# Performance work log

Measured on AMD Instinct MI355X. Metric: run time of the kernel, lower is better.

The kernel has to match this reference:

```python
import jax, jax.numpy as jnp
import numpy as np

HIDDEN = 768
INTER = 3072
HEADS = 12
HEAD_DIM = INTER // HEADS  # 256
LN_EPS = 1e-6
R_SOFTPLUS_0 = 1.442695041


def setup_inputs() -> dict:
    key = jax.random.key(0)
    ks = jax.random.split(key, 12)
    s = 0.02
    inp = {
        "hidden_states": jax.random.normal(ks[0], (8, 4096, HIDDEN), dtype=jnp.float32),
        "pooling_query": jax.random.normal(ks[1], (1, 1, HIDDEN), dtype=jnp.float32) * s,
        "Wq": jax.random.normal(ks[2], (HIDDEN, INTER), dtype=jnp.float32) * s,
        "bq": jnp.zeros((INTER,), dtype=jnp.float32),
        "Wk": jax.random.normal(ks[3], (HIDDEN, INTER), dtype=jnp.float32) * s,
        "bk": jnp.zeros((INTER,), dtype=jnp.float32),
        "Wv": jax.random.normal(ks[4], (HIDDEN, INTER), dtype=jnp.float32) * s,
        "bv": jnp.zeros((INTER,), dtype=jnp.float32),
        "Wp": jax.random.normal(ks[5], (INTER, HIDDEN), dtype=jnp.float32) * s,
        "bp": jnp.zeros((HIDDEN,), dtype=jnp.float32),
        "per_dim_scale": jnp.zeros((HEAD_DIM,), dtype=jnp.float32),
        "ln_w": jnp.ones((HIDDEN,), dtype=jnp.float32),
        "ln_b": jnp.zeros((HIDDEN,), dtype=jnp.float32),
    }
    return inp


def reference(hidden_states, pooling_query, Wq, bq, Wk, bk, Wv, bv, Wp, bp,
              per_dim_scale, ln_w, ln_b):
    B, S, _ = hidden_states.shape
    dt = hidden_states.dtype

    # Query: single pooling token, identical across batch -> [H, D]
    q = (pooling_query.reshape(1, HIDDEN) @ Wq + bq).reshape(HEADS, HEAD_DIM)
    # PerDimScale: q * (r_softplus0/sqrt(D)) * softplus(per_dim_scale)
    scale = (R_SOFTPLUS_0 / np.sqrt(HEAD_DIM)).astype(np.float32)
    q = q * (scale * jax.nn.softplus(per_dim_scale))

    # K/V projections: [B, S, H, D]
    k = (hidden_states @ Wk + bk).reshape(B, S, HEADS, HEAD_DIM)
    v = (hidden_states @ Wv + bv).reshape(B, S, HEADS, HEAD_DIM)

    # Single-query attention: logits [B, H, S]; scaling=1.0 (scale_logits_by_head_dims=False)
    # logit cap skipped (no_attention_logit_cap=True)
    logits = jnp.einsum("hd,bshd->bhs", q, k)
    attn = jax.nn.softmax(logits.astype(jnp.float32), axis=-1).astype(dt)

    # Weighted sum over seq: [B, H, D] -> concat heads -> [B, H*D]
    ctx = jnp.einsum("bhs,bshd->bhd", attn, v).reshape(B, HEADS * HEAD_DIM)

    out = ctx @ Wp + bp  # [B, HIDDEN]
    # LayerNorm; note the original forward adds ones to ln weight in-place each call,
    # so effective weight for one call is (ln_w + 1).
    mean = jnp.mean(out, axis=-1, keepdims=True)
    var = jnp.var(out, axis=-1, keepdims=True)
    out = (out - mean) * jax.lax.rsqrt(var + LN_EPS) * (ln_w + 1.0) + ln_b

    pooled = out[:, None, :]  # [B, 1, HIDDEN]
    attn_weights = attn[:, :, None, :]  # [B, H, 1, S]
    return pooled, attn_weights
```

## Files before the change

kernel.cpp:

```cpp
#include <hip/hip_runtime.h>
#include <cstdint>
#include <cmath>

#define LN_EPS 1e-6f

#define N_QCH 24u
#define O_QPART 0u
#define O_Q     73728u
#define O_WK    76800u
#define O_BKE   86016u
#define O_PHP   86032u
#define O_PLOG  O_PHP
#define N_SC    32
#define O_PH    (O_PHP + 2359296u)
#define O_CTXP  (O_PH + 73728u)
#define N_CCH   12
#define O_CTX   (O_CTXP + 294912u)
#define O_OUTP  (O_CTX + 24576u)
#define N_ICH   48

__device__ __forceinline__ float waveReduceSum(float v) {
#pragma unroll
    for (int o = 32; o >= 1; o >>= 1) v += __shfl_xor(v, o, 64);
    return v;
}
__device__ __forceinline__ float waveReduceMax(float v) {
#pragma unroll
    for (int o = 32; o >= 1; o >>= 1) v = fmaxf(v, __shfl_xor(v, o, 64));
    return v;
}

__global__ __launch_bounds__(256) void k1_qpart(const float* __restrict__ pq,
                                                const float* __restrict__ Wq,
                                                float* __restrict__ ws) {
    int h = blockIdx.x % 12;
    int ch = blockIdx.x / 12;
    int tid = threadIdx.x;
    int col = h * 256 + tid;
    int c0 = ch * 32;
    float acc = 0.f;
#pragma unroll 8
    for (int i = 0; i < 32; ++i) {
        int c = c0 + i;
        acc += pq[c] * Wq[c * 3072 + col];
    }
    ws[O_QPART + ch * 3072 + col] = acc;
}

__global__ __launch_bounds__(256) void k1b_qreduce(const float* __restrict__ bq,
                                                   const float* __restrict__ pds,
                                                   float* __restrict__ ws) {
    int j = blockIdx.x * 256 + threadIdx.x;
    float acc = bq[j];
#pragma unroll
    for (unsigned ch = 0; ch < N_QCH; ++ch) acc += ws[O_QPART + ch * 3072 + j];
    float x = pds[j & 255];
    float sp = (x > 20.f) ? x : log1pf(expf(x));
    const float scale = 1.442695041f / 16.0f;
    ws[O_Q + j] = acc * scale * sp;
}

__global__ __launch_bounds__(256) void k2_wkeff(const float* __restrict__ Wk,
                                                float* __restrict__ ws) {
    __shared__ float sh[4];
    int tid = threadIdx.x;
    int blk = blockIdx.x;
    int c = blk / 12, h = blk % 12;
    float v = Wk[c * 3072 + h * 256 + tid] * ws[O_Q + h * 256 + tid];
    v = waveReduceSum(v);
    if ((tid & 63) == 0) sh[tid >> 6] = v;
    __syncthreads();
    if (tid == 0) ws[O_WK + c * 12 + h] = sh[0] + sh[1] + sh[2] + sh[3];
}

__global__ __launch_bounds__(256) void k3_logits(const float* __restrict__ hidden,
                                                 float* __restrict__ ws) {
    __shared__ float4 tile4[1536];
    __shared__ float4 wkb4[288];
    int blk = blockIdx.x;
    int half = blk & 1;
    int st = (blk >> 1) & 63;
    int b = blk >> 7;
    int s0 = st * 64;
    const float* hb = hidden + (size_t)(b * 4096 + s0) * 768;
    const float4* wkg4 = reinterpret_cast<const float4*>(ws + O_WK);
    int tid = threadIdx.x;
    int w = tid >> 6, lane = tid & 63;
    float acc[12];
#pragma unroll
    for (int h = 0; h < 12; ++h) acc[h] = 0.f;

    for (int ch = 0; ch < 4; ++ch) {
        int cbase = half * 384 + ch * 96;
        __syncthreads();
        for (int i = tid; i < 288; i += 256) wkb4[i] = wkg4[cbase * 3 + i];
#pragma unroll
        for (int it = 0; it < 6; ++it) {
            int idx = it * 256 + tid;
            int r = idx / 24, j = idx % 24;
            const float4 v = *reinterpret_cast<const float4*>(hb + r * 768 + cbase + j * 4);
            tile4[r * 24 + (j ^ (r & 7))] = v;
        }
        __syncthreads();
#pragma unroll
        for (int jj = 0; jj < 6; ++jj) {
            int jcol = w * 6 + jj;
            float4 x = tile4[lane * 24 + (jcol ^ (lane & 7))];
            const float4* wr = &wkb4[jcol * 12];
            float xc[4] = {x.x, x.y, x.z, x.w};
#pragma unroll
            for (int cc = 0; cc < 4; ++cc) {
                float4 w0 = wr[cc * 3 + 0], w1 = wr[cc * 3 + 1], w2 = wr[cc * 3 + 2];
                acc[0] += xc[cc] * w0.x;  acc[1] += xc[cc] * w0.y;  acc[2]  += xc[cc] * w0.z;  acc[3]  += xc[cc] * w0.w;
                acc[4] += xc[cc] * w1.x;  acc[5] += xc[cc] * w1.y;  acc[6]  += xc[cc] * w1.z;  acc[7]  += xc[cc] * w1.w;
                acc[8] += xc[cc] * w2.x;  acc[9] += xc[cc] * w2.y;  acc[10] += xc[cc] * w2.z;  acc[11] += xc[cc] * w2.w;
            }
        }
    }
    __syncthreads();
    float* red = reinterpret_cast<float*>(tile4);
#pragma unroll
    for (int h = 0; h < 12; ++h) red[(w * 12 + h) * 64 + lane] = acc[h];
    __syncthreads();
    float* plog = ws + O_PLOG;
    for (int idx = tid; idx < 768; idx += 256) {
        int h = idx / 64, r = idx & 63;
        float v = red[(0 + h) * 64 + r] + red[(12 + h) * 64 + r] +
                  red[(24 + h) * 64 + r] + red[(36 + h) * 64 + r];
        plog[(size_t)half * 393216 + (size_t)(b * 12 + h) * 4096 + s0 + r] = v;
    }
}

__global__ __launch_bounds__(256) void k4_softmax(const float* __restrict__ ws,
                                                  float* __restrict__ attn) {
    __shared__ float sh[4];
    int row = blockIdx.x;
    const float4* p0 = reinterpret_cast<const float4*>(ws + O_PLOG + (size_t)row * 4096);
    const float4* p1 = reinterpret_cast<const float4*>(ws + O_PLOG + 393216u + (size_t)row * 4096);
    float* base = attn + (size_t)row * 4096;
    int tid = threadIdx.x;
    float4 x[4];
#pragma unroll
    for (int t = 0; t < 4; ++t) {
        float4 a = p0[t * 256 + tid], c = p1[t * 256 + tid];
        x[t].x = a.x + c.x; x[t].y = a.y + c.y; x[t].z = a.z + c.z; x[t].w = a.w + c.w;
    }
    float m = -1e30f;
#pragma unroll
    for (int t = 0; t < 4; ++t) {
        m = fmaxf(m, fmaxf(fmaxf(x[t].x, x[t].y), fmaxf(x[t].z, x[t].w)));
    }
    m = waveReduceMax(m);
    if ((tid & 63) == 0) sh[tid >> 6] = m;
    __syncthreads();
    m = fmaxf(fmaxf(sh[0], sh[1]), fmaxf(sh[2], sh[3]));
    __syncthreads();
    float s = 0.f;
#pragma unroll
    for (int t = 0; t < 4; ++t) {
        x[t].x = expf(x[t].x - m); x[t].y = expf(x[t].y - m);
        x[t].z = expf(x[t].z - m); x[t].w = expf(x[t].w - m);
        s += x[t].x + x[t].y + x[t].z + x[t].w;
    }
    s = waveReduceSum(s);
    if ((tid & 63) == 0) sh[tid >> 6] = s;
    __syncthreads();
    s = sh[0] + sh[1] + sh[2] + sh[3];
    float inv = 1.0f / s;
#pragma unroll
    for (int t = 0; t < 4; ++t) {
        x[t].x *= inv; x[t].y *= inv; x[t].z *= inv; x[t].w *= inv;
        reinterpret_cast<float4*>(base)[t * 256 + tid] = x[t];
    }
}

__global__ __launch_bounds__(256) void k5_phpart(const float* __restrict__ hidden,
                                                 const float* __restrict__ attn,
                                                 float* __restrict__ ws) {
    int blk = blockIdx.x;
    int sc = blk & 31;
    int ct = (blk >> 5) % 3;
    int b = blk / 96;
    int tid = threadIdx.x;
    int c = ct * 256 + tid;
    int s0 = sc * 128;
    const float* hb = hidden + (size_t)(b * 4096 + s0) * 768 + c;
    const float* ab = attn + (size_t)b * 49152 + s0;
    float acc[12];
#pragma unroll
    for (int h = 0; h < 12; ++h) acc[h] = 0.f;
    for (int g = 0; g < 32; ++g) {
        float x0 = hb[(g * 4 + 0) * 768];
        float x1 = hb[(g * 4 + 1) * 768];
        float x2 = hb[(g * 4 + 2) * 768];
        float x3 = hb[(g * 4 + 3) * 768];
#pragma unroll
        for (int h = 0; h < 12; ++h) {
            const float4 a = *reinterpret_cast<const float4*>(ab + h * 4096 + g * 4);
            acc[h] += a.x * x0 + a.y * x1 + a.z * x2 + a.w * x3;
        }
    }
    float* php = ws + O_PHP;
#pragma unroll
    for (int h = 0; h < 12; ++h)
        php[(size_t)(sc * 96 + b * 12 + h) * 768 + c] = acc[h];
}

__global__ __launch_bounds__(256) void k6_phreduce(float* __restrict__ ws) {
    int gid = blockIdx.x * 256 + threadIdx.x;
    const float* php = ws + O_PHP;
    float s = 0.f;
#pragma unroll
    for (int sc = 0; sc < N_SC; ++sc) s += php[(size_t)sc * 73728 + gid];
    ws[O_PH + gid] = s;
}

__global__ __launch_bounds__(256) void k7_ctxpart(const float* __restrict__ Wv,
                                                  float* __restrict__ ws) {
    int blk = blockIdx.x;
    int jt = blk % 12, cch = blk / 12;
    int tid = threadIdx.x;
    int j = jt * 256 + tid;
    int h = jt;
    const float* ph = ws + O_PH;
    float acc[8];
#pragma unroll
    for (int b = 0; b < 8; ++b) acc[b] = 0.f;
    for (int cc = 0; cc < 64; ++cc) {
        int c = cch * 64 + cc;
        float wv = Wv[(size_t)c * 3072 + j];
#pragma unroll
        for (int b = 0; b < 8; ++b) acc[b] += ph[(b * 12 + h) * 768 + c] * wv;
    }
#pragma unroll
    for (int b = 0; b < 8; ++b)
        ws[O_CTXP + (size_t)(cch * 8 + b) * 3072 + j] = acc[b];
}

__global__ __launch_bounds__(256) void k7b_ctxreduce(const float* __restrict__ bv,
                                                     float* __restrict__ ws) {
    int gid = blockIdx.x * 256 + threadIdx.x;
    int b = gid / 3072, i = gid % 3072;
    float s = bv[i];
#pragma unroll
    for (int cch = 0; cch < N_CCH; ++cch) s += ws[O_CTXP + (size_t)(cch * 8 + b) * 3072 + i];
    ws[O_CTX + gid] = s;
}

__global__ __launch_bounds__(256) void k8_outpart(const float* __restrict__ Wp,
                                                  float* __restrict__ ws) {
    int blk = blockIdx.x;
    int jt = blk % 3, ich = blk / 3;
    int tid = threadIdx.x;
    int j = jt * 256 + tid;
    const float* ctx = ws + O_CTX;
    float acc[8];
#pragma unroll
    for (int b = 0; b < 8; ++b) acc[b] = 0.f;
    for (int ii = 0; ii < 64; ++ii) {
        int i = ich * 64 + ii;
        float wp = Wp[(size_t)i * 768 + j];
#pragma unroll
        for (int b = 0; b < 8; ++b) acc[b] += ctx[b * 3072 + i] * wp;
    }
#pragma unroll
    for (int b = 0; b < 8; ++b)
        ws[O_OUTP + (size_t)(ich * 8 + b) * 768 + j] = acc[b];
}

__global__ __launch_bounds__(256) void k9_ln(const float* __restrict__ bp,
                                             const float* __restrict__ ln_w,
                                             const float* __restrict__ ln_b,
                                             const float* __restrict__ ws,
                                             float* __restrict__ pooled) {
    __shared__ float sh[8];
    int b = blockIdx.x, tid = threadIdx.x;
    const float* op = ws + O_OUTP;
    float vals[3];
    float lsum = 0.f, lsq = 0.f;
#pragma unroll
    for (int t = 0; t < 3; ++t) {
        int j = t * 256 + tid;
        float v = bp[j];
#pragma unroll
        for (int ich = 0; ich < N_ICH; ++ich) v += op[(size_t)(ich * 8 + b) * 768 + j];
        vals[t] = v; lsum += v; lsq += v * v;
    }
    lsum = waveReduceSum(lsum);
    lsq = waveReduceSum(lsq);
    if ((tid & 63) == 0) { sh[tid >> 6] = lsum; sh[4 + (tid >> 6)] = lsq; }
    __syncthreads();
    float mean = (sh[0] + sh[1] + sh[2] + sh[3]) * (1.f / 768.f);
    float var = (sh[4] + sh[5] + sh[6] + sh[7]) * (1.f / 768.f) - mean * mean;
    float inv = rsqrtf(var + LN_EPS);
#pragma unroll
    for (int t = 0; t < 3; ++t) {
        int j = t * 256 + tid;
        pooled[b * 768 + j] = (vals[t] - mean) * inv * (ln_w[j] + 1.f) + ln_b[j];
    }
}

extern "C" void kernel_launch(void* const* d_in, const int* in_sizes, int n_in,
                              void* d_out, int out_size, void* d_ws, size_t ws_size,
                              hipStream_t stream) {
    const float* hidden = (const float*)d_in[0];
    const float* pq     = (const float*)d_in[1];
    const float* Wq     = (const float*)d_in[2];
    const float* bq     = (const float*)d_in[3];
    const float* Wk     = (const float*)d_in[4];
    const float* bv     = (const float*)d_in[7];
    const float* Wv     = (const float*)d_in[6];
    const float* Wp     = (const float*)d_in[8];
    const float* bp     = (const float*)d_in[9];
    const float* pds    = (const float*)d_in[10];
    const float* ln_w   = (const float*)d_in[11];
    const float* ln_b   = (const float*)d_in[12];
    float* out = (float*)d_out;
    float* ws  = (float*)d_ws;
    float* pooled = out;
    float* attn   = out + 6144;

    k1_qpart   <<<288, 256, 0, stream>>>(pq, Wq, ws);
    k1b_qreduce<<<12, 256, 0, stream>>>(bq, pds, ws);
    k2_wkeff   <<<9216, 256, 0, stream>>>(Wk, ws);
    k3_logits  <<<1024, 256, 0, stream>>>(hidden, ws);
    k4_softmax <<<96, 256, 0, stream>>>(ws, attn);
    k5_phpart  <<<768, 256, 0, stream>>>(hidden, attn, ws);
    k6_phreduce<<<288, 256, 0, stream>>>(ws);
    k7_ctxpart <<<144, 256, 0, stream>>>(Wv, ws);
    k7b_ctxreduce<<<96, 256, 0, stream>>>(bv, ws);
    k8_outpart <<<144, 256, 0, stream>>>(Wp, ws);
    k9_ln      <<<8, 256, 0, stream>>>(bp, ln_w, ln_b, ws, pooled);
}
```

Measured before the change: 273.2 us.

## Split logits over four channel quarters with prefetched loads, vectorize phpart and wkeff

The logits kernel now splits the hidden dimension into four quarters across twice as many blocks. Each block issues all of its global loads up front into registers before staging them through shared memory, which raises memory-level parallelism. Softmax sums four partial logit buffers instead of two. The weighted-hidden partial kernel now uses float4 loads along channels, with waves splitting rows and a shared-memory reduction. The Wk-effective kernel is collapsed to one block per channel using float4 wave dot products. The costs are more partial-logit traffic and higher register pressure in the logits kernel.

Measured after the change: 282.9 us. +3.6%, slower.

```diff
diff --git a/kernel.cpp b/kernel.cpp
--- a/kernel.cpp
+++ b/kernel.cpp
@@ -8,15 +8,14 @@
 #define O_QPART 0u
 #define O_Q     73728u
 #define O_WK    76800u
-#define O_BKE   86016u
-#define O_PHP   86032u
-#define O_PLOG  O_PHP
+#define O_PLOG  86016u
+#define O_PHP   1658880u
 #define N_SC    32
-#define O_PH    (O_PHP + 2359296u)
-#define O_CTXP  (O_PH + 73728u)
+#define O_PH    4018176u
+#define O_CTXP  4091904u
 #define N_CCH   12
-#define O_CTX   (O_CTXP + 294912u)
-#define O_OUTP  (O_CTX + 24576u)
+#define O_CTX   4386816u
+#define O_OUTP  4411392u
 #define N_ICH   48
 
 __device__ __forceinline__ float waveReduceSum(float v) {
@@ -62,51 +61,67 @@
 
 __global__ __launch_bounds__(256) void k2_wkeff(const float* __restrict__ Wk,
                                                 float* __restrict__ ws) {
-    __shared__ float sh[4];
-    int tid = threadIdx.x;
+    int c = blockIdx.x;
+    int tid = threadIdx.x;
+    int w = tid >> 6, lane = tid & 63;
+    const float4* wk = reinterpret_cast<const float4*>(Wk + (size_t)c * 3072);
+    const float4* qv = reinterpret_cast<const float4*>(ws + O_Q);
+#pragma unroll
+    for (int i = 0; i < 3; ++i) {
+        int h = w * 3 + i;
+        float4 a = wk[h * 64 + lane];
+        float4 b = qv[h * 64 + lane];
+        float d = a.x * b.x + a.y * b.y + a.z * b.z + a.w * b.w;
+        d = waveReduceSum(d);
+        if (lane == 0) ws[O_WK + c * 12 + h] = d;
+    }
+}
+
+__global__ __launch_bounds__(256, 4) void k3_logits(const float* __restrict__ hidden,
+                                                    float* __restrict__ ws) {
+    __shared__ float4 tile4[1536];
+    __shared__ float4 wkb4[576];
     int blk = blockIdx.x;
-    int c = blk / 12, h = blk % 12;
-    float v = Wk[c * 3072 + h * 256 + tid] * ws[O_Q + h * 256 + tid];
-    v = waveReduceSum(v);
-    if ((tid & 63) == 0) sh[tid >> 6] = v;
-    __syncthreads();
-    if (tid == 0) ws[O_WK + c * 12 + h] = sh[0] + sh[1] + sh[2] + sh[3];
-}
-
-__global__ __launch_bounds__(256) void k3_logits(const float* __restrict__ hidden,
-                                                 float* __restrict__ ws) {
-    __shared__ float4 tile4[1536];
-    __shared__ float4 wkb4[288];
-    int blk = blockIdx.x;
-    int half = blk & 1;
-    int st = (blk >> 1) & 63;
-    int b = blk >> 7;
+    int q = blk & 3;
+    int st = (blk >> 2) & 63;
+    int b = blk >> 8;
     int s0 = st * 64;
     const float* hb = hidden + (size_t)(b * 4096 + s0) * 768;
     const float4* wkg4 = reinterpret_cast<const float4*>(ws + O_WK);
     int tid = threadIdx.x;
     int w = tid >> 6, lane = tid & 63;
+    int r = (6 * 256 + tid) / 24 - 64;
+    int rr[6], jj6[6];
+#pragma unroll
+    for (int it = 0; it < 6; ++it) {
+        int idx = it * 256 + tid;
+        rr[it] = idx / 24;
+        jj6[it] = idx % 24;
+    }
+    float4 v0[6], v1[6];
+#pragma unroll
+    for (int it = 0; it < 6; ++it)
+        v0[it] = reinterpret_cast<const float4*>(hb + rr[it] * 768 + q * 192)[jj6[it]];
+#pragma unroll
+    for (int it = 0; it < 6; ++it)
+        v1[it] = reinterpret_cast<const float4*>(hb + rr[it] * 768 + q * 192 + 96)[jj6[it]];
+    for (int i = tid; i < 576; i += 256) wkb4[i] = wkg4[q * 576 + i];
+
     float acc[12];
 #pragma unroll
     for (int h = 0; h < 12; ++h) acc[h] = 0.f;
 
-    for (int ch = 0; ch < 4; ++ch) {
-        int cbase = half * 384 + ch * 96;
-        __syncthreads();
-        for (int i = tid; i < 288; i += 256) wkb4[i] = wkg4[cbase * 3 + i];
-#pragma unroll
-        for (int it = 0; it < 6; ++it) {
-            int idx = it * 256 + tid;
-            int r = idx / 24, j = idx % 24;
-            const float4 v = *reinterpret_cast<const float4*>(hb + r * 768 + cbase + j * 4);
-            tile4[r * 24 + (j ^ (r & 7))] = v;
-        }
+#pragma unroll
+    for (int cph = 0; cph < 2; ++cph) {
+#pragma unroll
+        for (int it = 0; it < 6; ++it)
+            tile4[rr[it] * 24 + (jj6[it] ^ (rr[it] & 7))] = cph ? v1[it] : v0[it];
         __syncthreads();
 #pragma unroll
         for (int jj = 0; jj < 6; ++jj) {
             int jcol = w * 6 + jj;
             float4 x = tile4[lane * 24 + (jcol ^ (lane & 7))];
-            const float4* wr = &wkb4[jcol * 12];
+            const float4* wr = &wkb4[cph * 288 + jcol * 12];
             float xc[4] = {x.x, x.y, x.z, x.w};
 #pragma unroll
             for (int cc = 0; cc < 4; ++cc) {
@@ -116,19 +131,20 @@
                 acc[8] += xc[cc] * w2.x;  acc[9] += xc[cc] * w2.y;  acc[10] += xc[cc] * w2.z;  acc[11] += xc[cc] * w2.w;
             }
         }
-    }
-    __syncthreads();
+        __syncthreads();
+    }
     float* red = reinterpret_cast<float*>(tile4);
 #pragma unroll
     for (int h = 0; h < 12; ++h) red[(w * 12 + h) * 64 + lane] = acc[h];
     __syncthreads();
     float* plog = ws + O_PLOG;
     for (int idx = tid; idx < 768; idx += 256) {
-        int h = idx / 64, r = idx & 63;
-        float v = red[(0 + h) * 64 + r] + red[(12 + h) * 64 + r] +
-                  red[(24 + h) * 64 + r] + red[(36 + h) * 64 + r];
-        plog[(size_t)half * 393216 + (size_t)(b * 12 + h) * 4096 + s0 + r] = v;
-    }
+        int h = idx / 64, r2 = idx & 63;
+        float v = red[(0 + h) * 64 + r2] + red[(12 + h) * 64 + r2] +
+                  red[(24 + h) * 64 + r2] + red[(36 + h) * 64 + r2];
+        plog[(size_t)q * 393216 + (size_t)(b * 12 + h) * 4096 + s0 + r2] = v;
+    }
+    (void)r;
 }
 
 __global__ __launch_bounds__(256) void k4_softmax(const float* __restrict__ ws,
@@ -136,20 +152,25 @@
     __shared__ float sh[4];
     int row = blockIdx.x;
     const float4* p0 = reinterpret_cast<const float4*>(ws + O_PLOG + (size_t)row * 4096);
-    const float4* p1 = reinterpret_cast<const float4*>(ws + O_PLOG + 393216u + (size_t)row * 4096);
+    const float4* p1 = p0 + 98304;
+    const float4* p2 = p0 + 196608;
+    const float4* p3 = p0 + 294912;
     float* base = attn + (size_t)row * 4096;
     int tid = threadIdx.x;
     float4 x[4];
 #pragma unroll
     for (int t = 0; t < 4; ++t) {
         float4 a = p0[t * 256 + tid], c = p1[t * 256 + tid];
-        x[t].x = a.x + c.x; x[t].y = a.y + c.y; x[t].z = a.z + c.z; x[t].w = a.w + c.w;
+        float4 d = p2[t * 256 + tid], e = p3[t * 256 + tid];
+        x[t].x = (a.x + c.x) + (d.x + e.x);
+        x[t].y = (a.y + c.y) + (d.y + e.y);
+        x[t].z = (a.z + c.z) + (d.z + e.z);
+        x[t].w = (a.w + c.w) + (d.w + e.w);
     }
     float m = -1e30f;
 #pragma unroll
-    for (int t = 0; t < 4; ++t) {
+    for (int t = 0; t < 4; ++t)
         m = fmaxf(m, fmaxf(fmaxf(x[t].x, x[t].y), fmaxf(x[t].z, x[t].w)));
-    }
     m = waveReduceMax(m);
     if ((tid & 63) == 0) sh[tid >> 6] = m;
     __syncthreads();
@@ -177,33 +198,49 @@
 __global__ __launch_bounds__(256) void k5_phpart(const float* __restrict__ hidden,
                                                  const float* __restrict__ attn,
                                                  float* __restrict__ ws) {
+    __shared__ float4 sh4[12 * 4 * 64];
     int blk = blockIdx.x;
     int sc = blk & 31;
     int ct = (blk >> 5) % 3;
     int b = blk / 96;
     int tid = threadIdx.x;
-    int c = ct * 256 + tid;
+    int w = tid >> 6, lane = tid & 63;
+    int c = ct * 256 + lane * 4;
     int s0 = sc * 128;
     const float* hb = hidden + (size_t)(b * 4096 + s0) * 768 + c;
-    const float* ab = attn + (size_t)b * 49152 + s0;
-    float acc[12];
-#pragma unroll
-    for (int h = 0; h < 12; ++h) acc[h] = 0.f;
+    const float* ab = attn + (size_t)b * 49152 + s0 + w;
+    float4 acc[12];
+#pragma unroll
+    for (int h = 0; h < 12; ++h) acc[h] = make_float4(0.f, 0.f, 0.f, 0.f);
     for (int g = 0; g < 32; ++g) {
-        float x0 = hb[(g * 4 + 0) * 768];
-        float x1 = hb[(g * 4 + 1) * 768];
-        float x2 = hb[(g * 4 + 2) * 768];
-        float x3 = hb[(g * 4 + 3) * 768];
+        float4 x = *reinterpret_cast<const float4*>(hb + (size_t)(g * 4 + w) * 768);
+        float a[12];
+#pragma unroll
+        for (int h = 0; h < 12; ++h) a[h] = ab[h * 4096 + g * 4];
 #pragma unroll
         for (int h = 0; h < 12; ++h) {
-            const float4 a = *reinterpret_cast<const float4*>(ab + h * 4096 + g * 4);
-            acc[h] += a.x * x0 + a.y * x1 + a.z * x2 + a.w * x3;
+            acc[h].x += a[h] * x.x; acc[h].y += a[h] * x.y;
+            acc[h].z += a[h] * x.z; acc[h].w += a[h] * x.w;
         }
     }
+#pragma unroll
+    for (int h = 0; h < 12; ++h) sh4[(h * 4 + w) * 64 + lane] = acc[h];
+    __syncthreads();
     float* php = ws + O_PHP;
 #pragma unroll
-    for (int h = 0; h < 12; ++h)
-        php[(size_t)(sc * 96 + b * 12 + h) * 768 + c] = acc[h];
+    for (int i = 0; i < 3; ++i) {
+        int h = w * 3 + i;
+        float4 a = sh4[(h * 4 + 0) * 64 + lane];
+        float4 b2 = sh4[(h * 4 + 1) * 64 + lane];
+        float4 c2 = sh4[(h * 4 + 2) * 64 + lane];
+        float4 d = sh4[(h * 4 + 3) * 64 + lane];
+        float4 r;
+        r.x = (a.x + b2.x) + (c2.x + d.x);
+        r.y = (a.y + b2.y) + (c2.y + d.y);
+        r.z = (a.z + b2.z) + (c2.z + d.z);
+        r.w = (a.w + b2.w) + (c2.w + d.w);
+        *reinterpret_cast<float4*>(php + (size_t)(sc * 96 + b * 12 + h) * 768 + c) = r;
+    }
 }
 
 __global__ __launch_bounds__(256) void k6_phreduce(float* __restrict__ ws) {
@@ -308,8 +345,8 @@
     const float* Wq     = (const float*)d_in[2];
     const float* bq     = (const float*)d_in[3];
     const float* Wk     = (const float*)d_in[4];
+    const float* Wv     = (const float*)d_in[6];
     const float* bv     = (const float*)d_in[7];
-    const float* Wv     = (const float*)d_in[6];
     const float* Wp     = (const float*)d_in[8];
     const float* bp     = (const float*)d_in[9];
     const float* pds    = (const float*)d_in[10];
@@ -322,8 +359,8 @@
 
     k1_qpart   <<<288, 256, 0, stream>>>(pq, Wq, ws);
     k1b_qreduce<<<12, 256, 0, stream>>>(bq, pds, ws);
-    k2_wkeff   <<<9216, 256, 0, stream>>>(Wk, ws);
-    k3_logits  <<<1024, 256, 0, stream>>>(hidden, ws);
+    k2_wkeff   <<<768, 256, 0, stream>>>(Wk, ws);
+    k3_logits  <<<2048, 256, 0, stream>>>(hidden, ws);
     k4_softmax <<<96, 256, 0, stream>>>(ws, attn);
     k5_phpart  <<<768, 256, 0, stream>>>(hidden, attn, ws);
     k6_phreduce<<<288, 256, 0, stream>>>(ws);
```
